# Kernel optimization log

Hardware: AMD Instinct MI355X
Metric: run time of the kernel (lower is better)

Reference implementation:

```python
import jax, jax.numpy as jnp
import numpy as np

GROUP_SIZE = 128  # AWQ default quantization group size
PACK = 8


def dequant_awq(qweight, qzeros, scales, group_size=GROUP_SIZE):
    """Dequantize AWQ int4 weights.
    qweight: int32 [K, N//8], qzeros: int32 [G, N//8], scales: f32 [G, N]
    Returns f32 [K, N] with W = (q - z) * scale, per group of `group_size` rows.
    (Nibble layout here is sequential; the packed values are generated with the
    same layout in setup_inputs, so the math matches the AWQ kernel.)
    """
    K = qweight.shape[0]
    N = qweight.shape[1] * PACK
    shifts = (jnp.arange(PACK, dtype=jnp.int32) * 4)  # [8]
    # unpack 4-bit fields
    w = ((qweight[:, :, None] >> shifts) & 0xF).reshape(K, N)        # [K, N] int
    z = ((qzeros[:, :, None] >> shifts) & 0xF).reshape(-1, N)        # [G, N] int
    G = z.shape[0]
    w = w.reshape(G, group_size, N).astype(scales.dtype)             # [G, gs, N]
    W = (w - z[:, None, :].astype(scales.dtype)) * scales[:, None, :]
    return W.reshape(K, N)


def setup_inputs() -> dict:
    key = jax.random.key(0)
    ks = jax.random.split(key, 7)
    B, S, D, F = 4, 2048, 4096, 16384
    imin, imax = jnp.iinfo(jnp.int32).min, jnp.iinfo(jnp.int32).max
    return {
        "x": jax.random.normal(ks[0], (B, S, D), dtype=jnp.float32),
        "up_qweight": jax.random.randint(ks[1], (D, F // PACK), imin, imax, dtype=jnp.int32),
        "up_qzeros": jax.random.randint(ks[2], (D // GROUP_SIZE, F // PACK), imin, imax, dtype=jnp.int32),
        "up_scales": jax.random.uniform(ks[3], (D // GROUP_SIZE, F), dtype=jnp.float32, minval=0.001, maxval=0.02),
        "down_qweight": jax.random.randint(ks[4], (F, D // PACK), imin, imax, dtype=jnp.int32),
        "down_qzeros": jax.random.randint(ks[5], (F // GROUP_SIZE, D // PACK), imin, imax, dtype=jnp.int32),
        "down_scales": jax.random.uniform(ks[6], (F // GROUP_SIZE, D), dtype=jnp.float32, minval=0.001, maxval=0.02),
    }


def reference(x, up_qweight, up_qzeros, up_scales, down_qweight, down_qzeros, down_scales):
    xf = x.reshape(-1, x.shape[-1])                       # [T, D]
    W_up = dequant_awq(up_qweight, up_qzeros, up_scales)  # [D, F]
    h = jax.nn.gelu(xf @ W_up, approximate=False)         # [T, F]
    W_down = dequant_awq(down_qweight, down_qzeros, down_scales)  # [F, D]
    return h @ W_down                                     # [T, D]
```

## Files before the change

kernel.cpp:

```cpp
#include <hip/hip_runtime.h>

typedef __attribute__((ext_vector_type(8))) __bf16 bf16x8;
typedef __attribute__((ext_vector_type(4))) float f32x4;

#define DEV __device__ __forceinline__

DEV unsigned short f2bf(float f) {
  unsigned int u = __float_as_uint(f);
  u += 0x7FFFu + ((u >> 16) & 1u);
  return (unsigned short)(u >> 16);
}

__global__ __launch_bounds__(256) void k_f32_to_bf16(const float* __restrict__ x,
                                                     unsigned short* __restrict__ y) {
  size_t i = ((size_t)blockIdx.x * 256 + threadIdx.x) * 8;
  float4 a = *(const float4*)(x + i);
  float4 b = *(const float4*)(x + i + 4);
  union { unsigned short u[8]; uint4 v; } o;
  o.u[0] = f2bf(a.x); o.u[1] = f2bf(a.y); o.u[2] = f2bf(a.z); o.u[3] = f2bf(a.w);
  o.u[4] = f2bf(b.x); o.u[5] = f2bf(b.y); o.u[6] = f2bf(b.z); o.u[7] = f2bf(b.w);
  *(uint4*)(y + i) = o.v;
}

__global__ __launch_bounds__(256) void k_dequant_t(const int* __restrict__ qw,
                                                   const int* __restrict__ qz,
                                                   const float* __restrict__ sc,
                                                   unsigned short* __restrict__ wt,
                                                   int K, int N) {
  __shared__ __align__(16) unsigned short st[64][72];
  const int k0 = blockIdx.x * 64, n0 = blockIdx.y * 64;
  const int t = threadIdx.x;
  const int g = k0 >> 7;
  const int Np = N >> 3;
#pragma unroll
  for (int it = 0; it < 2; ++it) {
    int idx = t + it * 256;
    int k = idx >> 3;
    int nc = idx & 7;
    unsigned int w = (unsigned int)qw[(size_t)(k0 + k) * Np + (n0 >> 3) + nc];
    unsigned int z = (unsigned int)qz[(size_t)g * Np + (n0 >> 3) + nc];
#pragma unroll
    for (int i = 0; i < 8; ++i) {
      float s = sc[(size_t)g * N + n0 + nc * 8 + i];
      float v = ((float)(int)((w >> (4 * i)) & 0xFu) -
                 (float)(int)((z >> (4 * i)) & 0xFu)) * s;
      st[nc * 8 + i][k] = f2bf(v);
    }
  }
  __syncthreads();
  const int n = t >> 2, c = t & 3;
  uint4 v0 = *(const uint4*)&st[n][c * 16];
  uint4 v1 = *(const uint4*)&st[n][c * 16 + 8];
  unsigned short* dst = wt + (size_t)(n0 + n) * K + k0 + c * 16;
  *(uint4*)dst = v0;
  *(uint4*)(dst + 8) = v1;
}


#define STAGE_A(h) do { const unsigned short* g_ = A + gsA + (size_t)(h) * 32;               \
  __builtin_amdgcn_global_load_lds((const __attribute__((address_space(1))) void*)g_,        \
      (__attribute__((address_space(3))) void*)(&sA[(h) & 3][0] + tid * 8), 16, 0, 0);       \
  __builtin_amdgcn_global_load_lds((const __attribute__((address_space(1))) void*)(g_ + (size_t)128 * K), \
      (__attribute__((address_space(3))) void*)(&sA[(h) & 3][4096] + tid * 8), 16, 0, 0); } while (0)
#define STAGE_B(h) do { const unsigned short* g_ = B + gsB + (size_t)(h) * 32;               \
  __builtin_amdgcn_global_load_lds((const __attribute__((address_space(1))) void*)g_,        \
      (__attribute__((address_space(3))) void*)(&sB[(h) & 3][0] + tid * 8), 16, 0, 0);       \
  __builtin_amdgcn_global_load_lds((const __attribute__((address_space(1))) void*)(g_ + (size_t)128 * K), \
      (__attribute__((address_space(3))) void*)(&sB[(h) & 3][4096] + tid * 8), 16, 0, 0); } while (0)

#define LDA(s, m) (*(const bf16x8*)((const char*)&sA[s][0] + offA + (m) * 1024))
#define LDB(s, n) (*(const bf16x8*)((const char*)&sB[s][0] + offB + (n) * 1024))

template <int GELU>
__global__ __launch_bounds__(512, 2) void k_gemm256(const unsigned short* __restrict__ A,
                                                    const unsigned short* __restrict__ B,
                                                    void* __restrict__ C,
                                                    int M, int N, int K) {
  __shared__ __align__(16) unsigned short sA[4][8192];
  __shared__ __align__(16) unsigned short sB[4][8192];
  const int tid = threadIdx.x;
  const int lane = tid & 63;
  const int wave = tid >> 6;
  const int wm = wave >> 2, wn = wave & 3;
  const int r16 = lane & 15, q = lane >> 4;

  const int nbx = N >> 8;
  const int cpx = gridDim.x >> 3;
  const int g = (blockIdx.x & 7) * cpx + (blockIdx.x >> 3);
  const int gw = nbx << 4;
  const int grp = g / gw;
  const int rem = g - grp * gw;
  const int m0 = (grp * 16 + (rem & 15)) * 256;
  const int n0 = (rem >> 4) * 256;

  const int rA = wm * 128 + r16;
  const int rB = wn * 64 + r16;
  const int offA = rA * 64 + ((q * 16) ^ (((rA >> 1) & 3) << 4));
  const int offB = rB * 64 + ((q * 16) ^ (((rB >> 1) & 3) << 4));

  const int sr = tid >> 2;
  const int ssrc = (tid & 3) ^ ((sr >> 1) & 3);
  const size_t gsA = (size_t)(m0 + sr) * K + (size_t)ssrc * 8;
  const size_t gsB = (size_t)(n0 + sr) * K + (size_t)ssrc * 8;

  f32x4 acc[8][4] = {};
  bf16x8 pA0[8], pB0[4], pA1[8], pB1[4];
  const int NT = K >> 6;

  STAGE_A(0); STAGE_B(0); STAGE_A(1); STAGE_B(1);

  for (int t = 0; t < NT; ++t) {
    const int s0 = (2 * t) & 3, s1 = (2 * t + 1) & 3;

    asm volatile("s_waitcnt vmcnt(0)" ::: "memory");
    __builtin_amdgcn_s_barrier();

#pragma unroll
    for (int i = 0; i < 8; ++i) pA0[i] = LDA(s0, i);
#pragma unroll
    for (int j = 0; j < 4; ++j) pB0[j] = LDB(s0, j);
#pragma unroll
    for (int i = 0; i < 8; ++i) pA1[i] = LDA(s1, i);
#pragma unroll
    for (int j = 0; j < 4; ++j) pB1[j] = LDB(s1, j);

    if (t < NT - 1) {
      STAGE_A(2 * t + 2); STAGE_B(2 * t + 2);
      STAGE_A(2 * t + 3); STAGE_B(2 * t + 3);
    }

    __builtin_amdgcn_s_setprio(1);
#pragma unroll
    for (int i = 0; i < 8; ++i)
#pragma unroll
      for (int j = 0; j < 4; ++j)
        acc[i][j] = __builtin_amdgcn_mfma_f32_16x16x32_bf16(pA0[i], pB0[j], acc[i][j], 0, 0, 0);
#pragma unroll
    for (int i = 0; i < 8; ++i)
#pragma unroll
      for (int j = 0; j < 4; ++j)
        acc[i][j] = __builtin_amdgcn_mfma_f32_16x16x32_bf16(pA1[i], pB1[j], acc[i][j], 0, 0, 0);
    __builtin_amdgcn_s_setprio(0);
  }

  const int mb = m0 + wm * 128 + q * 4;
  const int nb = n0 + wn * 64 + r16;
#pragma unroll
  for (int i = 0; i < 8; ++i) {
#pragma unroll
    for (int j = 0; j < 4; ++j) {
#pragma unroll
      for (int r = 0; r < 4; ++r) {
        int row = mb + i * 16 + r;
        int col = nb + j * 16;
        float v = acc[i][j][r];
        if (GELU) {
          v = 0.5f * v * (1.0f + erff(v * 0.70710678118654752440f));
          ((unsigned short*)C)[(size_t)row * N + col] = f2bf(v);
        } else {
          ((float*)C)[(size_t)row * N + col] = v;
        }
      }
    }
  }
}

extern "C" void kernel_launch(void* const* d_in, const int* in_sizes, int n_in,
                              void* d_out, int out_size, void* d_ws, size_t ws_size,
                              hipStream_t stream) {
  const float* x  = (const float*)d_in[0];
  const int* uqw  = (const int*)d_in[1];
  const int* uqz  = (const int*)d_in[2];
  const float* usc = (const float*)d_in[3];
  const int* dqw  = (const int*)d_in[4];
  const int* dqz  = (const int*)d_in[5];
  const float* dsc = (const float*)d_in[6];
  float* out = (float*)d_out;

  const int T = 8192, D = 4096, F = 16384;
  char* ws = (char*)d_ws;
  unsigned short* xb = (unsigned short*)ws;
  unsigned short* h  = (unsigned short*)(ws + (size_t)T * D * 2);
  unsigned short* wt = (unsigned short*)(ws + (size_t)T * D * 2 + (size_t)T * F * 2);

  k_f32_to_bf16<<<dim3((T * D) / (256 * 8)), 256, 0, stream>>>(x, xb);
  k_dequant_t<<<dim3(D / 64, F / 64), 256, 0, stream>>>(uqw, uqz, usc, wt, D, F);
  k_gemm256<1><<<dim3((T / 256) * (F / 256)), 512, 0, stream>>>(xb, wt, (void*)h, T, F, D);
  k_dequant_t<<<dim3(F / 64, D / 64), 256, 0, stream>>>(dqw, dqz, dsc, wt, F, D);
  k_gemm256<0><<<dim3((T / 256) * (D / 256)), 512, 0, stream>>>(h, wt, (void*)out, T, D, F);
}
```

Measured before the change: 2.278 ms.

## Shrink GEMM tile to 128x256 with 4 waves and 3-stage software pipeline

Replaces the 256x256 tile, 8-wave GEMM with a 128x256 tile using 4 waves, each computing a 128x64 sub-tile. The LDS ring becomes a 3-slot buffer of 32-wide K slabs, and the fragment reads for the next slab are interleaved with the MFMAs on the current slab, with barriers every half step. The aim is to overlap LDS reads with MFMA work and raise occupancy and wave parallelism. In exchange, the smaller M tile lowers arithmetic intensity and adds global traffic for the B operand.

```diff
diff --git a/kernel.cpp b/kernel.cpp
--- a/kernel.cpp
+++ b/kernel.cpp
@@ -57,31 +57,45 @@
 }
 
 
-#define STAGE_A(h) do { const unsigned short* g_ = A + gsA + (size_t)(h) * 32;               \
+#define STAGE_A(h) do { const unsigned short* g_ = A + gsA + (size_t)(h) * 32; int sl_ = (h) % 3; \
   __builtin_amdgcn_global_load_lds((const __attribute__((address_space(1))) void*)g_,        \
-      (__attribute__((address_space(3))) void*)(&sA[(h) & 3][0] + tid * 8), 16, 0, 0);       \
+      (__attribute__((address_space(3))) void*)(&sA[sl_][0] + tid * 8), 16, 0, 0);           \
+  __builtin_amdgcn_global_load_lds((const __attribute__((address_space(1))) void*)(g_ + (size_t)64 * K), \
+      (__attribute__((address_space(3))) void*)(&sA[sl_][2048] + tid * 8), 16, 0, 0); } while (0)
+#define STAGE_B(h) do { const unsigned short* g_ = B + gsB + (size_t)(h) * 32; int sl_ = (h) % 3; \
+  __builtin_amdgcn_global_load_lds((const __attribute__((address_space(1))) void*)g_,        \
+      (__attribute__((address_space(3))) void*)(&sB[sl_][0] + tid * 8), 16, 0, 0);           \
+  __builtin_amdgcn_global_load_lds((const __attribute__((address_space(1))) void*)(g_ + (size_t)64 * K), \
+      (__attribute__((address_space(3))) void*)(&sB[sl_][2048] + tid * 8), 16, 0, 0);        \
   __builtin_amdgcn_global_load_lds((const __attribute__((address_space(1))) void*)(g_ + (size_t)128 * K), \
-      (__attribute__((address_space(3))) void*)(&sA[(h) & 3][4096] + tid * 8), 16, 0, 0); } while (0)
-#define STAGE_B(h) do { const unsigned short* g_ = B + gsB + (size_t)(h) * 32;               \
-  __builtin_amdgcn_global_load_lds((const __attribute__((address_space(1))) void*)g_,        \
-      (__attribute__((address_space(3))) void*)(&sB[(h) & 3][0] + tid * 8), 16, 0, 0);       \
-  __builtin_amdgcn_global_load_lds((const __attribute__((address_space(1))) void*)(g_ + (size_t)128 * K), \
-      (__attribute__((address_space(3))) void*)(&sB[(h) & 3][4096] + tid * 8), 16, 0, 0); } while (0)
+      (__attribute__((address_space(3))) void*)(&sB[sl_][4096] + tid * 8), 16, 0, 0);        \
+  __builtin_amdgcn_global_load_lds((const __attribute__((address_space(1))) void*)(g_ + (size_t)192 * K), \
+      (__attribute__((address_space(3))) void*)(&sB[sl_][6144] + tid * 8), 16, 0, 0); } while (0)
 
 #define LDA(s, m) (*(const bf16x8*)((const char*)&sA[s][0] + offA + (m) * 1024))
 #define LDB(s, n) (*(const bf16x8*)((const char*)&sB[s][0] + offB + (n) * 1024))
 
+#define READ_FRAGS(s, PA, PB) do {                                            \
+  _Pragma("unroll") for (int i_ = 0; i_ < 8; ++i_) PA[i_] = LDA(s, i_);       \
+  _Pragma("unroll") for (int j_ = 0; j_ < 4; ++j_) PB[j_] = LDB(s, j_); } while (0)
+
+#define MFMA_SLAB(PA, PB) do {                                                \
+  __builtin_amdgcn_s_setprio(1);                                              \
+  _Pragma("unroll") for (int i_ = 0; i_ < 8; ++i_)                            \
+    _Pragma("unroll") for (int j_ = 0; j_ < 4; ++j_)                          \
+      acc[i_][j_] = __builtin_amdgcn_mfma_f32_16x16x32_bf16(PA[i_], PB[j_], acc[i_][j_], 0, 0, 0); \
+  __builtin_amdgcn_s_setprio(0); } while (0)
+
 template <int GELU>
-__global__ __launch_bounds__(512, 2) void k_gemm256(const unsigned short* __restrict__ A,
+__global__ __launch_bounds__(256, 2) void k_gemm128(const unsigned short* __restrict__ A,
                                                     const unsigned short* __restrict__ B,
                                                     void* __restrict__ C,
                                                     int M, int N, int K) {
-  __shared__ __align__(16) unsigned short sA[4][8192];
-  __shared__ __align__(16) unsigned short sB[4][8192];
+  __shared__ __align__(16) unsigned short sA[3][4096];
+  __shared__ __align__(16) unsigned short sB[3][8192];
   const int tid = threadIdx.x;
   const int lane = tid & 63;
   const int wave = tid >> 6;
-  const int wm = wave >> 2, wn = wave & 3;
   const int r16 = lane & 15, q = lane >> 4;
 
   const int nbx = N >> 8;
@@ -90,12 +104,11 @@
   const int gw = nbx << 4;
   const int grp = g / gw;
   const int rem = g - grp * gw;
-  const int m0 = (grp * 16 + (rem & 15)) * 256;
+  const int m0 = (grp * 16 + (rem & 15)) * 128;
   const int n0 = (rem >> 4) * 256;
 
-  const int rA = wm * 128 + r16;
-  const int rB = wn * 64 + r16;
-  const int offA = rA * 64 + ((q * 16) ^ (((rA >> 1) & 3) << 4));
+  const int rB = wave * 64 + r16;
+  const int offA = r16 * 64 + ((q * 16) ^ (((r16 >> 1) & 3) << 4));
   const int offB = rB * 64 + ((q * 16) ^ (((rB >> 1) & 3) << 4));
 
   const int sr = tid >> 2;
@@ -105,46 +118,31 @@
 
   f32x4 acc[8][4] = {};
   bf16x8 pA0[8], pB0[4], pA1[8], pB1[4];
-  const int NT = K >> 6;
+  const int NT2 = K >> 5;
 
-  STAGE_A(0); STAGE_B(0); STAGE_A(1); STAGE_B(1);
+  STAGE_A(0); STAGE_B(0); STAGE_A(1); STAGE_B(1); STAGE_A(2); STAGE_B(2);
+  asm volatile("s_waitcnt vmcnt(0)" ::: "memory");
+  __builtin_amdgcn_s_barrier();
+  READ_FRAGS(0, pA0, pB0);
 
-  for (int t = 0; t < NT; ++t) {
-    const int s0 = (2 * t) & 3, s1 = (2 * t + 1) & 3;
+  for (int i = 0; i < NT2; i += 2) {
+    const int s1 = (i + 1) % 3, s2 = (i + 2) % 3;
 
-    asm volatile("s_waitcnt vmcnt(0)" ::: "memory");
+    asm volatile("s_waitcnt vmcnt(0) lgkmcnt(0)" ::: "memory");
     __builtin_amdgcn_s_barrier();
+    if (i + 3 < NT2) { STAGE_A(i + 3); STAGE_B(i + 3); }
+    READ_FRAGS(s1, pA1, pB1);
+    MFMA_SLAB(pA0, pB0);
 
-#pragma unroll
-    for (int i = 0; i < 8; ++i) pA0[i] = LDA(s0, i);
-#pragma unroll
-    for (int j = 0; j < 4; ++j) pB0[j] = LDB(s0, j);
-#pragma unroll
-    for (int i = 0; i < 8; ++i) pA1[i] = LDA(s1, i);
-#pragma unroll
-    for (int j = 0; j < 4; ++j) pB1[j] = LDB(s1, j);
-
-    if (t < NT - 1) {
-      STAGE_A(2 * t + 2); STAGE_B(2 * t + 2);
-      STAGE_A(2 * t + 3); STAGE_B(2 * t + 3);
-    }
-
-    __builtin_amdgcn_s_setprio(1);
-#pragma unroll
-    for (int i = 0; i < 8; ++i)
-#pragma unroll
-      for (int j = 0; j < 4; ++j)
-        acc[i][j] = __builtin_amdgcn_mfma_f32_16x16x32_bf16(pA0[i], pB0[j], acc[i][j], 0, 0, 0);
-#pragma unroll
-    for (int i = 0; i < 8; ++i)
-#pragma unroll
-      for (int j = 0; j < 4; ++j)
-        acc[i][j] = __builtin_amdgcn_mfma_f32_16x16x32_bf16(pA1[i], pB1[j], acc[i][j], 0, 0, 0);
-    __builtin_amdgcn_s_setprio(0);
+    asm volatile("s_waitcnt lgkmcnt(0)" ::: "memory");
+    __builtin_amdgcn_s_barrier();
+    if (i + 4 < NT2) { STAGE_A(i + 4); STAGE_B(i + 4); }
+    if (i + 2 < NT2) READ_FRAGS(s2, pA0, pB0);
+    MFMA_SLAB(pA1, pB1);
   }
 
-  const int mb = m0 + wm * 128 + q * 4;
-  const int nb = n0 + wn * 64 + r16;
+  const int mb = m0 + q * 4;
+  const int nb = n0 + wave * 64 + r16;
 #pragma unroll
   for (int i = 0; i < 8; ++i) {
 #pragma unroll
@@ -185,7 +183,7 @@
 
   k_f32_to_bf16<<<dim3((T * D) / (256 * 8)), 256, 0, stream>>>(x, xb);
   k_dequant_t<<<dim3(D / 64, F / 64), 256, 0, stream>>>(uqw, uqz, usc, wt, D, F);
-  k_gemm256<1><<<dim3((T / 256) * (F / 256)), 512, 0, stream>>>(xb, wt, (void*)h, T, F, D);
+  k_gemm128<1><<<dim3((T / 128) * (F / 256)), 256, 0, stream>>>(xb, wt, (void*)h, T, F, D);
   k_dequant_t<<<dim3(F / 64, D / 64), 256, 0, stream>>>(dqw, dqz, dsc, wt, F, D);
-  k_gemm256<0><<<dim3((T / 256) * (D / 256)), 512, 0, stream>>>(h, wt, (void*)out, T, D, F);
+  k_gemm128<0><<<dim3((T / 128) * (D / 256)), 256, 0, stream>>>(h, wt, (void*)out, T, D, F);
 }
```

Result: slower. 2.725 ms (+19.6%).
